# Optimization experiments

Hardware: AMD Instinct MI355X
Metric: run time of the kernel (lower is better)

## Reference

```python
import jax, jax.numpy as jnp
import numpy as np

B, S, HID = 2, 2048, 2048
H, HKV, D = 16, 4, 128
BS = 64            # block_size
TAU = 0.5          # threshold_tau
NB = S // BS       # number of blocks
SCALE = 1.0 / (D ** 0.5)


def _rotate_half(x):
    x1, x2 = x[..., : D // 2], x[..., D // 2 :]
    return jnp.concatenate([-x2, x1], axis=-1)


def setup_inputs() -> dict:
    key = jax.random.key(0)
    k0, k1, k2, k3, k4 = jax.random.split(key, 5)
    hidden_states = jax.random.normal(k0, (B, S, HID), jnp.float32)
    # standard rotary embeddings, [B, S, D] (ndim==3 path of _apply_rotary_pos_emb)
    pos = jnp.arange(S, dtype=jnp.float32)
    inv_freq = 1.0 / (10000.0 ** (jnp.arange(0, D, 2, dtype=jnp.float32) / D))
    emb = jnp.concatenate([pos[:, None] * inv_freq[None, :]] * 2, axis=-1)  # [S, D]
    cos = jnp.broadcast_to(jnp.cos(emb)[None], (B, S, D)).astype(jnp.float32)
    sin = jnp.broadcast_to(jnp.sin(emb)[None], (B, S, D)).astype(jnp.float32)
    Wq = jax.random.normal(k1, (HID, H * D), jnp.float32) * 0.02
    Wk = jax.random.normal(k2, (HID, HKV * D), jnp.float32) * 0.02
    Wv = jax.random.normal(k3, (HID, HKV * D), jnp.float32) * 0.02
    Wo = jax.random.normal(k4, (HID, HID), jnp.float32) * 0.02
    return {"hidden_states": hidden_states, "cos": cos, "sin": sin,
            "Wq": Wq, "Wk": Wk, "Wv": Wv, "Wo": Wo}


def reference(hidden_states, cos, sin, Wq, Wk, Wv, Wo):
    # QKV projections -> [B, heads, S, D]
    q = (hidden_states @ Wq).reshape(B, S, H, D).transpose(0, 2, 1, 3)
    k = (hidden_states @ Wk).reshape(B, S, HKV, D).transpose(0, 2, 1, 3)
    v = (hidden_states @ Wv).reshape(B, S, HKV, D).transpose(0, 2, 1, 3)
    # RoPE (cos/sin [B,S,D] -> broadcast over heads)
    c, s = cos[:, None], sin[:, None]
    q = q * c + _rotate_half(q) * s
    k = k * c + _rotate_half(k) * s
    # GQA repeat_interleave on head dim
    n_rep = H // HKV
    k = jnp.repeat(k, n_rep, axis=1)
    v = jnp.repeat(v, n_rep, axis=1)
    # ---- AttnGate: block-mean pooled Q/K scores -> hard block mask ----
    q_blk = q.reshape(B, H, NB, BS, D).mean(axis=3)  # [B,H,NB,D]
    k_blk = k.reshape(B, H, NB, BS, D).mean(axis=3)
    gate_logits = jnp.einsum('bhid,bhjd->bhij', q_blk, k_blk) * SCALE
    hard = jax.nn.sigmoid(gate_logits) >= TAU                      # [B,H,NB,NB]
    hard = hard | jnp.eye(NB, dtype=bool)                          # keep diagonal blocks
    hard = hard & jnp.tril(jnp.ones((NB, NB), dtype=bool))         # block-causal
    # expand block mask to token level and intersect with causal mask
    tok_mask = jnp.repeat(jnp.repeat(hard, BS, axis=2), BS, axis=3)  # [B,H,S,S]
    tok_mask = tok_mask & jnp.tril(jnp.ones((S, S), dtype=bool))
    # ---- block-sparse (masked) attention ----
    scores = jnp.einsum('bhsd,bhtd->bhst', q, k) * SCALE
    scores = jnp.where(tok_mask, scores, jnp.float32(-1e30))
    probs = jax.nn.softmax(scores.astype(jnp.float32), axis=-1).astype(v.dtype)
    out = jnp.einsum('bhst,bhtd->bhsd', probs, v)
    out = out.transpose(0, 2, 1, 3).reshape(B, S, HID)
    return out @ Wo
```

## Files before the change

kernel.cpp:

```cpp
#include <hip/hip_runtime.h>
#include <stdint.h>

typedef unsigned short u16;
typedef _Float16 half8 __attribute__((ext_vector_type(8)));
typedef float floatx4 __attribute__((ext_vector_type(4)));
typedef u16 u16x4 __attribute__((ext_vector_type(4)));

#define B_ 2
#define S_ 2048
#define HID_ 2048
#define H_ 16
#define HKV_ 4
#define D_ 128
#define NB_ 32
#define SCALE_ 0.08838834764831845f
#define SC_L2 0.12753102331884178f
#define SMAX_L2 5.770780163555852f

__device__ __forceinline__ u16 f2h_bits(float f) {
  _Float16 h = (_Float16)f;
  return __builtin_bit_cast(u16, h);
}

__global__ __launch_bounds__(256) void k_split_hs(const float* __restrict__ hs, u16* __restrict__ A2) {
  int idx = blockIdx.x * 256 + threadIdx.x;
  int f0 = idx * 4;
  float4 v = *reinterpret_cast<const float4*>(hs + f0);
  float vv[4] = {v.x, v.y, v.z, v.w};
  u16x4 h0, h1;
#pragma unroll
  for (int e = 0; e < 4; ++e) {
    _Float16 a = (_Float16)vv[e];
    float r = vv[e] - (float)a;
    _Float16 b = (_Float16)r;
    h0[e] = __builtin_bit_cast(u16, a);
    h1[e] = __builtin_bit_cast(u16, b);
  }
  int row = f0 >> 11;
  int col = f0 & 2047;
  *reinterpret_cast<u16x4*>(A2 + (size_t)row * 4096 + col) = h0;
  *reinterpret_cast<u16x4*>(A2 + (size_t)row * 4096 + 2048 + col) = h1;
}

__global__ __launch_bounds__(256) void k_transpose_split(const float* __restrict__ src, u16* __restrict__ dst,
                                                         int Kdim, int N, int ldd, int nsplit) {
  __shared__ float tile[64][65];
  int k0 = blockIdx.x * 64, n0 = blockIdx.y * 64;
#pragma unroll
  for (int p = 0; p < 16; ++p) {
    int e = threadIdx.x + p * 256;
    int r = e >> 6, c = e & 63;
    tile[r][c] = src[(size_t)(k0 + r) * N + n0 + c];
  }
  __syncthreads();
#pragma unroll
  for (int p = 0; p < 16; ++p) {
    int e = threadIdx.x + p * 256;
    int k = e & 63, n = e >> 6;
    float v = tile[k][n];
    for (int s = 0; s < nsplit; ++s) {
      _Float16 hh = (_Float16)v;
      dst[(size_t)(n0 + n) * ldd + s * Kdim + k0 + k] = __builtin_bit_cast(u16, hh);
      v -= (float)hh;
    }
  }
}

__global__ __launch_bounds__(256) void k_add(float4* __restrict__ out, const float4* __restrict__ p1) {
  size_t i = (size_t)blockIdx.x * 256 + threadIdx.x;
  float4 a = out[i], b = p1[i];
  out[i] = (float4){a.x + b.x, a.y + b.y, a.z + b.z, a.w + b.w};
}


#define FENCE() __builtin_amdgcn_sched_barrier(0)
#define BAR() do { FENCE(); __builtin_amdgcn_s_barrier(); FENCE(); } while (0)
#define WAITVM(N) do { FENCE(); asm volatile("s_waitcnt vmcnt(" #N ")" ::: "memory"); FENCE(); } while (0)

__device__ __forceinline__ int kmap(int map, int t) {
  return ((map >> ((t >> 5) * 4)) & 15) * 2048 + (t & 31) * 64;
}

__device__ __forceinline__ void stage_half(const u16* __restrict__ src, int sr0, int lda, int kb,
                                           u16* dst, int w, int lane) {
#pragma unroll
  for (int rr = 0; rr < 2; ++rr) {
    int chunk = rr * 8 + w;
    int row = chunk * 8 + (lane >> 3);
    int slot = (lane & 7) ^ (lane >> 3);
    const u16* gp = src + (size_t)(sr0 + row) * lda + kb + slot * 8;
    __builtin_amdgcn_global_load_lds((const __attribute__((address_space(1))) unsigned int*)gp,
                                     (__attribute__((address_space(3))) unsigned int*)(dst + chunk * 512),
                                     16, 0, 0);
  }
}

#define RD_A(mh) do { \
  _Pragma("unroll") \
  for (int m_ = 0; m_ < 4; ++m_) { \
    aF[m_][0] = *reinterpret_cast<const half8*>(&sm[(mh)*8192 + (wm*64 + m_*16 + l15)*64 + ((quad ^ l7) * 8)]); \
    aF[m_][1] = *reinterpret_cast<const half8*>(&sm[(mh)*8192 + (wm*64 + m_*16 + l15)*64 + (((4 + quad) ^ l7) * 8)]); \
  } } while (0)

#define RD_B(nh, BF) do { \
  _Pragma("unroll") \
  for (int n_ = 0; n_ < 2; ++n_) { \
    BF[n_][0] = *reinterpret_cast<const half8*>(&sm[16384 + (nh)*8192 + (wn*32 + n_*16 + l15)*64 + ((quad ^ l7) * 8)]); \
    BF[n_][1] = *reinterpret_cast<const half8*>(&sm[16384 + (nh)*8192 + (wn*32 + n_*16 + l15)*64 + (((4 + quad) ^ l7) * 8)]); \
  } } while (0)

#define MM(mh, nh, BF) do { \
  __builtin_amdgcn_s_setprio(1); \
  _Pragma("unroll") \
  for (int m_ = 0; m_ < 4; ++m_) \
  _Pragma("unroll") \
  for (int n_ = 0; n_ < 2; ++n_) { \
    acc[(mh)*4 + m_][(nh)*2 + n_] = __builtin_amdgcn_mfma_f32_16x16x32_f16(aF[m_][0], BF[n_][0], acc[(mh)*4 + m_][(nh)*2 + n_], 0, 0, 0); \
    acc[(mh)*4 + m_][(nh)*2 + n_] = __builtin_amdgcn_mfma_f32_16x16x32_f16(aF[m_][1], BF[n_][1], acc[(mh)*4 + m_][(nh)*2 + n_], 0, 0, 0); \
  } \
  __builtin_amdgcn_s_setprio(0); } while (0)

__device__ __forceinline__ void gemm256(const u16* __restrict__ A, const u16* __restrict__ BT,
                                        float* __restrict__ C, u16* __restrict__ Ch, u16* sm,
                                        int row0, int col0, int NT,
                                        int lda, int ldb, int ldc, int ldch,
                                        int amap, int bmap, int koffA, int koffB) {
  const int tid = (int)threadIdx.x;
  const int lane = tid & 63;
  const int w = tid >> 6;
  const int wm = w >> 2, wn = w & 3;
  const int quad = lane >> 4, l15 = lane & 15, l7 = lane & 7;

  floatx4 acc[8][4];
#pragma unroll
  for (int i = 0; i < 8; ++i)
#pragma unroll
    for (int j = 0; j < 4; ++j) acc[i][j] = (floatx4){0.f, 0.f, 0.f, 0.f};

  half8 aF[4][2], bF0[2][2], bF1[2][2];

  {
    int ka = kmap(amap, 0) + koffA, kb = kmap(bmap, 0) + koffB;
    stage_half(A,  row0,       lda, ka, sm + 0,     w, lane);
    stage_half(BT, col0,       ldb, kb, sm + 16384, w, lane);
    stage_half(BT, col0 + 128, ldb, kb, sm + 24576, w, lane);
    stage_half(A,  row0 + 128, lda, ka, sm + 8192,  w, lane);
  }
  WAITVM(4);
  BAR();

  for (int t = 0; t < NT; ++t) {
    int tn = t + 1; if (tn >= NT) tn = 0;
    int kan = kmap(amap, tn) + koffA, kbn = kmap(bmap, tn) + koffB;

    RD_A(0); RD_B(0, bF0);
    WAITVM(2);
    BAR(); MM(0, 0, bF0); BAR();
    RD_B(1, bF1);
    stage_half(A,  row0, lda, kan, sm + 0,     w, lane);
    stage_half(BT, col0, ldb, kbn, sm + 16384, w, lane);
    WAITVM(4);
    BAR(); MM(0, 1, bF1); BAR();
    RD_A(1);
    stage_half(BT, col0 + 128, ldb, kbn, sm + 24576, w, lane);
    BAR(); MM(1, 1, bF1); BAR();
    stage_half(A, row0 + 128, lda, kan, sm + 8192, w, lane);
    WAITVM(4);
    BAR(); MM(1, 0, bF0); BAR();
  }
  WAITVM(0);

#pragma unroll
  for (int i = 0; i < 8; ++i) {
    int mh = i >> 2, m = i & 3;
#pragma unroll
    for (int j = 0; j < 4; ++j) {
      int nh = j >> 1, n = j & 1;
#pragma unroll
      for (int r = 0; r < 4; ++r) {
        int rr = row0 + mh * 128 + wm * 64 + m * 16 + quad * 4 + r;
        int cc = col0 + nh * 128 + wn * 32 + n * 16 + l15;
        if (Ch)
          Ch[(size_t)rr * ldch + cc] = f2h_bits(acc[i][j][r]);
        else
          C[(size_t)rr * ldc + cc] = acc[i][j][r];
      }
    }
  }
}

__global__ __launch_bounds__(512) void k_gemm_qkv(const u16* __restrict__ A2, const u16* __restrict__ B2T,
                                                  const u16* __restrict__ WvT, float* __restrict__ qkv,
                                                  u16* __restrict__ corr) {
  __shared__ u16 sm[32768];
  int id = blockIdx.x;
  if (id < 160) {
    int row0 = (id / 10) * 256, col0 = (id % 10) * 256;
    gemm256(A2, B2T, nullptr, corr, sm, row0, col0, 64, 4096, 4096, 0, 2560, 0x01, 0x10, 0, 0);
  } else if (id < 320) {
    int t = id - 160;
    int row0 = (t / 10) * 256, col0 = (t % 10) * 256;
    gemm256(A2, B2T, qkv, nullptr, sm, row0, col0, 32, 4096, 4096, 3072, 0, 0, 0, 0, 0);
  } else {
    int t = id - 320;
    int row0 = (t >> 1) * 256, col0 = (t & 1) * 256;
    gemm256(A2, WvT, qkv + 2560, nullptr, sm, row0, col0, 32, 4096, 2048, 3072, 0, 0, 0, 0, 0);
  }
}

__global__ __launch_bounds__(512) void k_gemm_wo(const u16* __restrict__ attn, const u16* __restrict__ WoT,
                                                 float* __restrict__ out, float* __restrict__ P1) {
  __shared__ u16 sm[32768];
  int id = blockIdx.x;
  int p = id >> 7, rem = id & 127;
  int row0 = (rem >> 3) * 256, col0 = (rem & 7) * 256;
  float* Cp = p ? P1 : out;
  gemm256(attn, WoT, Cp, nullptr, sm, row0, col0, 16, 2048, 2048, 2048, 0, 0, 0,
          p * 1024, p * 1024);
}

__global__ __launch_bounds__(256) void k_rope_mean(const float* __restrict__ qkv, const u16* __restrict__ corr,
                                                   const float* __restrict__ cosb, const float* __restrict__ sinb,
                                                   u16* __restrict__ qbf, u16* __restrict__ kbf,
                                                   float* __restrict__ qblk, float* __restrict__ kblk) {
  int cc = blockIdx.x, i = blockIdx.y, b = blockIdx.z;
  int c = cc * 256 + threadIdx.x;
  bool isq = c < 2048;
  int hh = isq ? (c >> 7) : ((c - 2048) >> 7);
  int d = isq ? (c & 127) : ((c - 2048) & 127);
  int pairc = (d < 64) ? c + 64 : c - 64;
  float sgn = (d < 64) ? -1.0f : 1.0f;
  int row0 = b * S_ + i * 64;
  float sum = 0.0f;
  for (int s = 0; s < 64; ++s) {
    int row = row0 + s;
    float x1 = qkv[(size_t)row * 3072 + c]
             + (float)__builtin_bit_cast(_Float16, corr[(size_t)row * 2560 + c]);
    float x2 = qkv[(size_t)row * 3072 + pairc]
             + (float)__builtin_bit_cast(_Float16, corr[(size_t)row * 2560 + pairc]);
    float cv = cosb[(size_t)row * 128 + d];
    float sv = sinb[(size_t)row * 128 + d];
    float val = x1 * cv + sgn * x2 * sv;
    sum += val;
    if (isq)
      qbf[((size_t)(b * H_ + hh) * S_ + i * 64 + s) * 128 + d] = f2h_bits(val);
    else
      kbf[((size_t)(b * HKV_ + hh) * S_ + i * 64 + s) * 128 + d] = f2h_bits(val);
  }
  if (isq)
    qblk[((size_t)(b * H_ + hh) * NB_ + i) * 128 + d] = sum * 0.015625f;
  else
    kblk[((size_t)(b * HKV_ + hh) * NB_ + i) * 128 + d] = sum * 0.015625f;
}

__global__ __launch_bounds__(256) void k_vlayout(const float* __restrict__ qkv, u16* __restrict__ vT) {
  int i = blockIdx.x, hk = blockIdx.y, b = blockIdx.z;
  __shared__ u16 tile[64 * 130];
#pragma unroll
  for (int p = 0; p < 32; ++p) {
    int e = threadIdx.x + p * 256;
    int s = e >> 7, d = e & 127;
    float v = qkv[(size_t)(b * S_ + i * 64 + s) * 3072 + 2560 + hk * 128 + d];
    tile[s * 130 + d] = f2h_bits(v);
  }
  __syncthreads();
#pragma unroll
  for (int p = 0; p < 32; ++p) {
    int e = threadIdx.x + p * 256;
    int d2 = e >> 6, s2 = e & 63;
    vT[((size_t)(b * HKV_ + hk) * 128 + d2) * S_ + i * 64 + s2] = tile[s2 * 130 + d2];
  }
}

__global__ __launch_bounds__(256) void k_gate(const float* __restrict__ qblk, const float* __restrict__ kblk,
                                              int* __restrict__ mask) {
  int h = blockIdx.x, b = blockIdx.y;
  int hk = h >> 2;
  __shared__ float qs[32 * 128];
  __shared__ float ks[32 * 128];
  size_t qb0 = (size_t)(b * H_ + h) * NB_ * 128;
  size_t kb0 = (size_t)(b * HKV_ + hk) * NB_ * 128;
#pragma unroll
  for (int p = 0; p < 16; ++p) {
    int e = threadIdx.x + p * 256;
    qs[e] = qblk[qb0 + e];
    ks[e] = kblk[kb0 + e];
  }
  __syncthreads();
#pragma unroll
  for (int p = 0; p < 4; ++p) {
    int l = threadIdx.x + p * 256;
    int i = l >> 5, j = l & 31;
    int m;
    if (j > i) m = 0;
    else if (j == i) m = 1;
    else {
      float dot = 0.0f;
      for (int d = 0; d < 128; ++d) dot += qs[i * 128 + d] * ks[j * 128 + d];
      m = (dot >= 0.0f) ? 1 : 0;
    }
    mask[((size_t)(b * H_ + h) * NB_ + i) * NB_ + j] = m;
  }
}

__global__ __launch_bounds__(256) void k_flash(const u16* __restrict__ qbf, const u16* __restrict__ kbf,
                                               const u16* __restrict__ vT, const int* __restrict__ mask,
                                               u16* __restrict__ attn) {
  const int id = blockIdx.x;
  const int i = id >> 5;
  const int hb = id & 31;
  const int h = hb & 15, b = hb >> 4;
  const int hk = h >> 2;
  const int tid = threadIdx.x;
  const int lane = tid & 63;
  const int w = tid >> 6;
  const int quad = lane >> 4;
  const int l15 = lane & 15;

  __shared__ u16 Ks[64 * 128];
  __shared__ u16 Vs[128 * 64];
  __shared__ u16 Ps[4 * 16 * 64];

  half8 qF[4];
  const u16* qbase = qbf + ((size_t)(b * H_ + h) * S_ + i * 64 + w * 16 + l15) * 128;
#pragma unroll
  for (int kk = 0; kk < 4; ++kk)
    qF[kk] = *reinterpret_cast<const half8*>(qbase + kk * 32 + quad * 8);

  floatx4 o[8];
#pragma unroll
  for (int t = 0; t < 8; ++t) o[t] = (floatx4){0.f, 0.f, 0.f, 0.f};
  float ls[4] = {0.f, 0.f, 0.f, 0.f};

  const u16* kb = kbf + (size_t)(b * HKV_ + hk) * S_ * 128;
  const u16* vb = vT + (size_t)(b * HKV_ + hk) * 128 * S_;
  const int* mrp = mask + ((size_t)(b * H_ + h) * NB_ + i) * NB_;

  for (int j = 0; j <= i; ++j) {
    if (!mrp[j]) continue;
#pragma unroll
    for (int t = 0; t < 4; ++t) {
      int g2 = t * 4 + w;
      int stok = g2 * 4 + (lane >> 4);
      int ul = (lane & 15) ^ (stok & 15);
      const u16* srcK = kb + (size_t)(j * 64 + stok) * 128 + ul * 8;
      __builtin_amdgcn_global_load_lds((const __attribute__((address_space(1))) unsigned int*)srcK,
                                       (__attribute__((address_space(3))) unsigned int*)(Ks + g2 * 512),
                                       16, 0, 0);
      int sdd = g2 * 8 + (lane >> 3);
      int ulv = (lane & 7) ^ (sdd & 7);
      const u16* srcV = vb + (size_t)sdd * S_ + j * 64 + ulv * 8;
      __builtin_amdgcn_global_load_lds((const __attribute__((address_space(1))) unsigned int*)srcV,
                                       (__attribute__((address_space(3))) unsigned int*)(Vs + g2 * 512),
                                       16, 0, 0);
    }
    __syncthreads();

#pragma unroll
    for (int ct = 0; ct < 4; ++ct) {
      floatx4 cacc = (floatx4){0.f, 0.f, 0.f, 0.f};
#pragma unroll
      for (int kk = 0; kk < 4; ++kk) {
        int phys = (kk * 4 + quad) ^ l15;
        half8 bF = *reinterpret_cast<const half8*>(&Ks[(ct * 16 + l15) * 128 + phys * 8]);
        cacc = __builtin_amdgcn_mfma_f32_16x16x32_f16(qF[kk], bF, cacc, 0, 0, 0);
      }
#pragma unroll
      for (int r = 0; r < 4; ++r) {
        float s = cacc[r];
        if (j == i && (ct * 16 + l15) > (w * 16 + quad * 4 + r)) s = -1e30f;
        float p = __builtin_exp2f(fmaf(s, SC_L2, -SMAX_L2));
        _Float16 ph = (_Float16)p;
        ls[r] += (float)ph;
        Ps[w * 1024 + (quad * 4 + r) * 64 + ct * 16 + l15] = __builtin_bit_cast(u16, ph);
      }
    }
#pragma unroll
    for (int kk2 = 0; kk2 < 2; ++kk2) {
      half8 aP = *reinterpret_cast<const half8*>(&Ps[w * 1024 + l15 * 64 + kk2 * 32 + quad * 8]);
#pragma unroll
      for (int ct2 = 0; ct2 < 8; ++ct2) {
        int phys = (kk2 * 4 + quad) ^ (l15 & 7);
        half8 bV = *reinterpret_cast<const half8*>(&Vs[(ct2 * 16 + l15) * 64 + phys * 8]);
        o[ct2] = __builtin_amdgcn_mfma_f32_16x16x32_f16(aP, bV, o[ct2], 0, 0, 0);
      }
    }
    __syncthreads();
  }

#pragma unroll
  for (int xm = 1; xm < 16; xm <<= 1)
#pragma unroll
    for (int r = 0; r < 4; ++r) ls[r] += __shfl_xor(ls[r], xm, 64);
  float invl[4];
#pragma unroll
  for (int r = 0; r < 4; ++r) invl[r] = 1.0f / ls[r];
#pragma unroll
  for (int ct2 = 0; ct2 < 8; ++ct2)
#pragma unroll
    for (int r = 0; r < 4; ++r) {
      size_t row = (size_t)(b * S_ + i * 64 + w * 16 + quad * 4 + r);
      attn[row * 2048 + h * 128 + ct2 * 16 + l15] = f2h_bits(o[ct2][r] * invl[r]);
    }
}

extern "C" void kernel_launch(void* const* d_in, const int* in_sizes, int n_in,
                              void* d_out, int out_size, void* d_ws, size_t ws_size,
                              hipStream_t stream) {
  const float* hs = (const float*)d_in[0];
  const float* cosb = (const float*)d_in[1];
  const float* sinb = (const float*)d_in[2];
  const float* Wq = (const float*)d_in[3];
  const float* Wk = (const float*)d_in[4];
  const float* Wv = (const float*)d_in[5];
  const float* Wo = (const float*)d_in[6];
  float* out = (float*)d_out;
  char* ws = (char*)d_ws;

  u16* A2 = (u16*)(ws + 0);
  u16* B2T = (u16*)(ws + 33554432);
  u16* WvT = (u16*)(ws + 54525952);
  float* qkv = (float*)(ws + 56623104);
  u16* corr = (u16*)out;
  u16* attn = (u16*)(ws + 0);
  u16* qbf = (u16*)(ws + 16777216);
  u16* kbf = (u16*)(ws + 33554432);
  u16* vTbf = (u16*)(ws + 37748736);
  float* qblk = (float*)(ws + 41943040);
  float* kblk = (float*)(ws + 42467328);
  int* mask = (int*)(ws + 42598400);
  u16* WoT = (u16*)(ws + 43122688);
  float* P1 = (float*)(ws + 56623104);

  (void)in_sizes; (void)n_in; (void)out_size; (void)ws_size;

  k_split_hs<<<8192, 256, 0, stream>>>(hs, A2);
  k_transpose_split<<<dim3(32, 32), 256, 0, stream>>>(Wq, B2T, 2048, 2048, 4096, 2);
  k_transpose_split<<<dim3(32, 8), 256, 0, stream>>>(Wk, B2T + (size_t)2048 * 4096, 2048, 512, 4096, 2);
  k_transpose_split<<<dim3(32, 8), 256, 0, stream>>>(Wv, WvT, 2048, 512, 2048, 1);

  k_gemm_qkv<<<352, 512, 0, stream>>>(A2, B2T, WvT, qkv, corr);

  k_transpose_split<<<dim3(32, 32), 256, 0, stream>>>(Wo, WoT, 2048, 2048, 2048, 1);

  k_rope_mean<<<dim3(10, 32, 2), 256, 0, stream>>>(qkv, corr, cosb, sinb, qbf, kbf, qblk, kblk);
  k_vlayout<<<dim3(32, 4, 2), 256, 0, stream>>>(qkv, vTbf);

  k_gate<<<dim3(16, 2), 256, 0, stream>>>(qblk, kblk, mask);

  k_flash<<<1024, 256, 0, stream>>>(qbf, kbf, vTbf, mask, attn);

  k_gemm_wo<<<256, 512, 0, stream>>>(attn, WoT, out, P1);
  k_add<<<8192, 256, 0, stream>>>((float4*)out, (const float4*)P1);
}
```

Measured before the change: 422.4 us.

## Double-buffer LDS in GEMM main loop with one barrier per k-step

```diff
diff --git a/kernel.cpp b/kernel.cpp
--- a/kernel.cpp
+++ b/kernel.cpp
@@ -95,18 +95,18 @@
   }
 }
 
-#define RD_A(mh) do { \
+#define RD_A(RB, mh) do { \
   _Pragma("unroll") \
   for (int m_ = 0; m_ < 4; ++m_) { \
-    aF[m_][0] = *reinterpret_cast<const half8*>(&sm[(mh)*8192 + (wm*64 + m_*16 + l15)*64 + ((quad ^ l7) * 8)]); \
-    aF[m_][1] = *reinterpret_cast<const half8*>(&sm[(mh)*8192 + (wm*64 + m_*16 + l15)*64 + (((4 + quad) ^ l7) * 8)]); \
+    aF[m_][0] = *reinterpret_cast<const half8*>(&sm[(RB) + (mh)*8192 + (wm*64 + m_*16 + l15)*64 + ((quad ^ l7) * 8)]); \
+    aF[m_][1] = *reinterpret_cast<const half8*>(&sm[(RB) + (mh)*8192 + (wm*64 + m_*16 + l15)*64 + (((4 + quad) ^ l7) * 8)]); \
   } } while (0)
 
-#define RD_B(nh, BF) do { \
+#define RD_B(RB, nh, BF) do { \
   _Pragma("unroll") \
   for (int n_ = 0; n_ < 2; ++n_) { \
-    BF[n_][0] = *reinterpret_cast<const half8*>(&sm[16384 + (nh)*8192 + (wn*32 + n_*16 + l15)*64 + ((quad ^ l7) * 8)]); \
-    BF[n_][1] = *reinterpret_cast<const half8*>(&sm[16384 + (nh)*8192 + (wn*32 + n_*16 + l15)*64 + (((4 + quad) ^ l7) * 8)]); \
+    BF[n_][0] = *reinterpret_cast<const half8*>(&sm[(RB) + 16384 + (nh)*8192 + (wn*32 + n_*16 + l15)*64 + ((quad ^ l7) * 8)]); \
+    BF[n_][1] = *reinterpret_cast<const half8*>(&sm[(RB) + 16384 + (nh)*8192 + (wn*32 + n_*16 + l15)*64 + (((4 + quad) ^ l7) * 8)]); \
   } } while (0)
 
 #define MM(mh, nh, BF) do { \
@@ -120,6 +120,19 @@
   } \
   __builtin_amdgcn_s_setprio(0); } while (0)
 
+#define ITER(tcur, RB, SB) do { \
+  int tn = (tcur) + 1; if (tn >= NT) tn = 0; \
+  int kan = kmap(amap, tn) + koffA, kbn = kmap(bmap, tn) + koffB; \
+  stage_half(A,  row0,       lda, kan, sm + (SB) + 0,     w, lane); \
+  stage_half(A,  row0 + 128, lda, kan, sm + (SB) + 8192,  w, lane); \
+  stage_half(BT, col0,       ldb, kbn, sm + (SB) + 16384, w, lane); \
+  stage_half(BT, col0 + 128, ldb, kbn, sm + (SB) + 24576, w, lane); \
+  RD_A(RB, 0); RD_B(RB, 0, bF0); MM(0, 0, bF0); \
+  RD_B(RB, 1, bF1); MM(0, 1, bF1); \
+  RD_A(RB, 1); MM(1, 1, bF1); MM(1, 0, bF0); \
+  WAITVM(0); BAR(); \
+} while (0)
+
 __device__ __forceinline__ void gemm256(const u16* __restrict__ A, const u16* __restrict__ BT,
                                         float* __restrict__ C, u16* __restrict__ Ch, u16* sm,
                                         int row0, int col0, int NT,
@@ -142,33 +155,17 @@
   {
     int ka = kmap(amap, 0) + koffA, kb = kmap(bmap, 0) + koffB;
     stage_half(A,  row0,       lda, ka, sm + 0,     w, lane);
+    stage_half(A,  row0 + 128, lda, ka, sm + 8192,  w, lane);
     stage_half(BT, col0,       ldb, kb, sm + 16384, w, lane);
     stage_half(BT, col0 + 128, ldb, kb, sm + 24576, w, lane);
-    stage_half(A,  row0 + 128, lda, ka, sm + 8192,  w, lane);
-  }
-  WAITVM(4);
+  }
+  WAITVM(0);
   BAR();
 
-  for (int t = 0; t < NT; ++t) {
-    int tn = t + 1; if (tn >= NT) tn = 0;
-    int kan = kmap(amap, tn) + koffA, kbn = kmap(bmap, tn) + koffB;
-
-    RD_A(0); RD_B(0, bF0);
-    WAITVM(2);
-    BAR(); MM(0, 0, bF0); BAR();
-    RD_B(1, bF1);
-    stage_half(A,  row0, lda, kan, sm + 0,     w, lane);
-    stage_half(BT, col0, ldb, kbn, sm + 16384, w, lane);
-    WAITVM(4);
-    BAR(); MM(0, 1, bF1); BAR();
-    RD_A(1);
-    stage_half(BT, col0 + 128, ldb, kbn, sm + 24576, w, lane);
-    BAR(); MM(1, 1, bF1); BAR();
-    stage_half(A, row0 + 128, lda, kan, sm + 8192, w, lane);
-    WAITVM(4);
-    BAR(); MM(1, 0, bF0); BAR();
-  }
-  WAITVM(0);
+  for (int t = 0; t < NT; t += 2) {
+    ITER(t,     0,     32768);
+    ITER(t + 1, 32768, 0);
+  }
 
 #pragma unroll
   for (int i = 0; i < 8; ++i) {
@@ -192,7 +189,7 @@
 __global__ __launch_bounds__(512) void k_gemm_qkv(const u16* __restrict__ A2, const u16* __restrict__ B2T,
                                                   const u16* __restrict__ WvT, float* __restrict__ qkv,
                                                   u16* __restrict__ corr) {
-  __shared__ u16 sm[32768];
+  __shared__ u16 sm[65536];
   int id = blockIdx.x;
   if (id < 160) {
     int row0 = (id / 10) * 256, col0 = (id % 10) * 256;
@@ -210,7 +207,7 @@
 
 __global__ __launch_bounds__(512) void k_gemm_wo(const u16* __restrict__ attn, const u16* __restrict__ WoT,
                                                  float* __restrict__ out, float* __restrict__ P1) {
-  __shared__ u16 sm[32768];
+  __shared__ u16 sm[65536];
   int id = blockIdx.x;
   int p = id >> 7, rem = id & 127;
   int row0 = (rem >> 3) * 256, col0 = (rem & 7) * 256;
```

Measured after the change: 443.2 us. 1.05x slower.

## Double-buffer K/V tiles in flash kernel, reverse block order, fuse prep kernels

Applied to the files above, without the earlier changes.

```diff
diff --git a/kernel.cpp b/kernel.cpp
--- a/kernel.cpp
+++ b/kernel.cpp
@@ -22,30 +22,9 @@
   return __builtin_bit_cast(u16, h);
 }
 
-__global__ __launch_bounds__(256) void k_split_hs(const float* __restrict__ hs, u16* __restrict__ A2) {
-  int idx = blockIdx.x * 256 + threadIdx.x;
-  int f0 = idx * 4;
-  float4 v = *reinterpret_cast<const float4*>(hs + f0);
-  float vv[4] = {v.x, v.y, v.z, v.w};
-  u16x4 h0, h1;
-#pragma unroll
-  for (int e = 0; e < 4; ++e) {
-    _Float16 a = (_Float16)vv[e];
-    float r = vv[e] - (float)a;
-    _Float16 b = (_Float16)r;
-    h0[e] = __builtin_bit_cast(u16, a);
-    h1[e] = __builtin_bit_cast(u16, b);
-  }
-  int row = f0 >> 11;
-  int col = f0 & 2047;
-  *reinterpret_cast<u16x4*>(A2 + (size_t)row * 4096 + col) = h0;
-  *reinterpret_cast<u16x4*>(A2 + (size_t)row * 4096 + 2048 + col) = h1;
-}
-
-__global__ __launch_bounds__(256) void k_transpose_split(const float* __restrict__ src, u16* __restrict__ dst,
-                                                         int Kdim, int N, int ldd, int nsplit) {
-  __shared__ float tile[64][65];
-  int k0 = blockIdx.x * 64, n0 = blockIdx.y * 64;
+__device__ __forceinline__ void transpose_body(const float* __restrict__ src, u16* __restrict__ dst,
+                                               int Kdim, int N, int ldd, int nsplit,
+                                               int k0, int n0, float (*tile)[65]) {
 #pragma unroll
   for (int p = 0; p < 16; ++p) {
     int e = threadIdx.x + p * 256;
@@ -64,6 +43,48 @@
       v -= (float)hh;
     }
   }
+}
+
+__global__ __launch_bounds__(256) void k_prep(const float* __restrict__ hs, u16* __restrict__ A2,
+                                              const float* __restrict__ Wq, const float* __restrict__ Wk,
+                                              const float* __restrict__ Wv,
+                                              u16* __restrict__ B2T, u16* __restrict__ WvT) {
+  __shared__ float tile[64][65];
+  int id = blockIdx.x;
+  if (id < 8192) {
+    int idx = id * 256 + threadIdx.x;
+    int f0 = idx * 4;
+    float4 v = *reinterpret_cast<const float4*>(hs + f0);
+    float vv[4] = {v.x, v.y, v.z, v.w};
+    u16x4 h0, h1;
+#pragma unroll
+    for (int e = 0; e < 4; ++e) {
+      _Float16 a = (_Float16)vv[e];
+      float r = vv[e] - (float)a;
+      _Float16 b = (_Float16)r;
+      h0[e] = __builtin_bit_cast(u16, a);
+      h1[e] = __builtin_bit_cast(u16, b);
+    }
+    int row = f0 >> 11;
+    int col = f0 & 2047;
+    *reinterpret_cast<u16x4*>(A2 + (size_t)row * 4096 + col) = h0;
+    *reinterpret_cast<u16x4*>(A2 + (size_t)row * 4096 + 2048 + col) = h1;
+  } else if (id < 9216) {
+    int t = id - 8192;
+    transpose_body(Wq, B2T, 2048, 2048, 4096, 2, (t & 31) * 64, (t >> 5) * 64, tile);
+  } else if (id < 9472) {
+    int t = id - 9216;
+    transpose_body(Wk, B2T + (size_t)2048 * 4096, 2048, 512, 4096, 2, (t & 31) * 64, (t >> 5) * 64, tile);
+  } else {
+    int t = id - 9472;
+    transpose_body(Wv, WvT, 2048, 512, 2048, 1, (t & 31) * 64, (t >> 5) * 64, tile);
+  }
+}
+
+__global__ __launch_bounds__(256) void k_transpose_split(const float* __restrict__ src, u16* __restrict__ dst,
+                                                         int Kdim, int N, int ldd, int nsplit) {
+  __shared__ float tile[64][65];
+  transpose_body(src, dst, Kdim, N, ldd, nsplit, blockIdx.x * 64, blockIdx.y * 64, tile);
 }
 
 __global__ __launch_bounds__(256) void k_add(float4* __restrict__ out, const float4* __restrict__ p1) {
@@ -307,7 +328,7 @@
                                                const u16* __restrict__ vT, const int* __restrict__ mask,
                                                u16* __restrict__ attn) {
   const int id = blockIdx.x;
-  const int i = id >> 5;
+  const int i = 31 - (id >> 5);
   const int hb = id & 31;
   const int h = hb & 15, b = hb >> 4;
   const int hk = h >> 2;
@@ -317,8 +338,8 @@
   const int quad = lane >> 4;
   const int l15 = lane & 15;
 
-  __shared__ u16 Ks[64 * 128];
-  __shared__ u16 Vs[128 * 64];
+  __shared__ u16 Ksb[2 * 64 * 128];
+  __shared__ u16 Vsb[2 * 128 * 64];
   __shared__ u16 Ps[4 * 16 * 64];
 
   half8 qF[4];
@@ -336,39 +357,52 @@
   const u16* vb = vT + (size_t)(b * HKV_ + hk) * 128 * S_;
   const int* mrp = mask + ((size_t)(b * H_ + h) * NB_ + i) * NB_;
 
-  for (int j = 0; j <= i; ++j) {
-    if (!mrp[j]) continue;
-#pragma unroll
-    for (int t = 0; t < 4; ++t) {
-      int g2 = t * 4 + w;
-      int stok = g2 * 4 + (lane >> 4);
-      int ul = (lane & 15) ^ (stok & 15);
-      const u16* srcK = kb + (size_t)(j * 64 + stok) * 128 + ul * 8;
-      __builtin_amdgcn_global_load_lds((const __attribute__((address_space(1))) unsigned int*)srcK,
-                                       (__attribute__((address_space(3))) unsigned int*)(Ks + g2 * 512),
-                                       16, 0, 0);
-      int sdd = g2 * 8 + (lane >> 3);
-      int ulv = (lane & 7) ^ (sdd & 7);
-      const u16* srcV = vb + (size_t)sdd * S_ + j * 64 + ulv * 8;
-      __builtin_amdgcn_global_load_lds((const __attribute__((address_space(1))) unsigned int*)srcV,
-                                       (__attribute__((address_space(3))) unsigned int*)(Vs + g2 * 512),
-                                       16, 0, 0);
-    }
-    __syncthreads();
-
+#define FSTAGE(J, BUF) do { \
+  _Pragma("unroll") \
+  for (int t_ = 0; t_ < 4; ++t_) { \
+    int g2 = t_ * 4 + w; \
+    int stok = g2 * 4 + (lane >> 4); \
+    int ul = (lane & 15) ^ (stok & 15); \
+    const u16* srcK = kb + (size_t)((J) * 64 + stok) * 128 + ul * 8; \
+    __builtin_amdgcn_global_load_lds((const __attribute__((address_space(1))) unsigned int*)srcK, \
+                                     (__attribute__((address_space(3))) unsigned int*)(Ksb + (BUF) * 8192 + g2 * 512), \
+                                     16, 0, 0); \
+    int sdd = g2 * 8 + (lane >> 3); \
+    int ulv = (lane & 7) ^ (sdd & 7); \
+    const u16* srcV = vb + (size_t)sdd * S_ + (J) * 64 + ulv * 8; \
+    __builtin_amdgcn_global_load_lds((const __attribute__((address_space(1))) unsigned int*)srcV, \
+                                     (__attribute__((address_space(3))) unsigned int*)(Vsb + (BUF) * 8192 + g2 * 512), \
+                                     16, 0, 0); \
+  } } while (0)
+
+  int jcur = 0;
+  while (!mrp[jcur]) ++jcur;
+  FSTAGE(jcur, 0);
+  int cur = 0;
+
+  for (;;) {
+    int jn = jcur + 1;
+    while (jn <= i && !mrp[jn]) ++jn;
+    bool hn = (jn <= i);
+    if (hn) { FSTAGE(jn, cur ^ 1); WAITVM(8); }
+    else    { WAITVM(0); }
+    BAR();
+
+    const u16* Kc = Ksb + cur * 8192;
+    const u16* Vc = Vsb + cur * 8192;
 #pragma unroll
     for (int ct = 0; ct < 4; ++ct) {
       floatx4 cacc = (floatx4){0.f, 0.f, 0.f, 0.f};
 #pragma unroll
       for (int kk = 0; kk < 4; ++kk) {
         int phys = (kk * 4 + quad) ^ l15;
-        half8 bF = *reinterpret_cast<const half8*>(&Ks[(ct * 16 + l15) * 128 + phys * 8]);
+        half8 bF = *reinterpret_cast<const half8*>(&Kc[(ct * 16 + l15) * 128 + phys * 8]);
         cacc = __builtin_amdgcn_mfma_f32_16x16x32_f16(qF[kk], bF, cacc, 0, 0, 0);
       }
 #pragma unroll
       for (int r = 0; r < 4; ++r) {
         float s = cacc[r];
-        if (j == i && (ct * 16 + l15) > (w * 16 + quad * 4 + r)) s = -1e30f;
+        if (jcur == i && (ct * 16 + l15) > (w * 16 + quad * 4 + r)) s = -1e30f;
         float p = __builtin_exp2f(fmaf(s, SC_L2, -SMAX_L2));
         _Float16 ph = (_Float16)p;
         ls[r] += (float)ph;
@@ -381,11 +415,13 @@
 #pragma unroll
       for (int ct2 = 0; ct2 < 8; ++ct2) {
         int phys = (kk2 * 4 + quad) ^ (l15 & 7);
-        half8 bV = *reinterpret_cast<const half8*>(&Vs[(ct2 * 16 + l15) * 64 + phys * 8]);
+        half8 bV = *reinterpret_cast<const half8*>(&Vc[(ct2 * 16 + l15) * 64 + phys * 8]);
         o[ct2] = __builtin_amdgcn_mfma_f32_16x16x32_f16(aP, bV, o[ct2], 0, 0, 0);
       }
     }
-    __syncthreads();
+    BAR();
+    if (!hn) break;
+    jcur = jn; cur ^= 1;
   }
 
 #pragma unroll
@@ -434,10 +470,7 @@
 
   (void)in_sizes; (void)n_in; (void)out_size; (void)ws_size;
 
-  k_split_hs<<<8192, 256, 0, stream>>>(hs, A2);
-  k_transpose_split<<<dim3(32, 32), 256, 0, stream>>>(Wq, B2T, 2048, 2048, 4096, 2);
-  k_transpose_split<<<dim3(32, 8), 256, 0, stream>>>(Wk, B2T + (size_t)2048 * 4096, 2048, 512, 4096, 2);
-  k_transpose_split<<<dim3(32, 8), 256, 0, stream>>>(Wv, WvT, 2048, 512, 2048, 1);
+  k_prep<<<9728, 256, 0, stream>>>(hs, A2, Wq, Wk, Wv, B2T, WvT);
 
   k_gemm_qkv<<<352, 512, 0, stream>>>(A2, B2T, WvT, qkv, corr);
 
```

Measured after the change: 405.0 us. 4.1% less time.
